# Performance work log

Hardware: AMD Instinct MI355X
Metric: run time of the kernel (lower is better)

The kernel has to match this reference:

```python
import jax, jax.numpy as jnp
import numpy as np

L, D, H, DK, DV, DFF = 6, 512, 8, 64, 64, 2048
B, S = 8, 512
EPS = 1e-5


def _pos_table(max_len, d_model):
    pos = np.arange(max_len)[:, None].astype(np.float64)
    i = np.arange(d_model)[None, :].astype(np.float64)
    t = pos / np.power(10000.0, 2.0 * i / d_model)
    t[0, :] = 0.0
    t[1:, 0::2] = np.sin(t[1:, 0::2])
    t[1:, 1::2] = np.cos(t[1:, 1::2])
    return jnp.asarray(t, dtype=jnp.float32)


def _ln(x, g, b):
    m = jnp.mean(x, axis=-1, keepdims=True)
    v = jnp.mean(jnp.square(x - m), axis=-1, keepdims=True)
    return (x - m) * jax.lax.rsqrt(v + EPS) * g + b


def setup_inputs() -> dict:
    key = jax.random.key(0)
    ks = jax.random.split(key, 12)
    s = 0.02
    return {
        "enc_inputs": jax.random.normal(ks[0], (B, S, D), jnp.float32),
        "enc_inputs_mask": jax.random.randint(ks[1], (B, S), 0, 100, dtype=jnp.int64),
        "Wq": jax.random.normal(ks[2], (L, D, H * DK), jnp.float32) * s,
        "Wk": jax.random.normal(ks[3], (L, D, H * DK), jnp.float32) * s,
        "Wv": jax.random.normal(ks[4], (L, D, H * DV), jnp.float32) * s,
        "Wo": jax.random.normal(ks[5], (L, H * DV, D), jnp.float32) * s,
        "ln1_g": jnp.ones((L, D), jnp.float32),
        "ln1_b": jnp.zeros((L, D), jnp.float32),
        "W1": jax.random.normal(ks[6], (L, D, DFF), jnp.float32) * s,
        "W2": jax.random.normal(ks[7], (L, DFF, D), jnp.float32) * s,
        "ln2_g": jnp.ones((L, D), jnp.float32),
        "ln2_b": jnp.zeros((L, D), jnp.float32),
    }


def reference(enc_inputs, enc_inputs_mask, Wq, Wk, Wv, Wo, ln1_g, ln1_b, W1, W2, ln2_g, ln2_b):
    b, s, _ = enc_inputs.shape
    x = enc_inputs + _pos_table(s, D)  # positional encoding (dropout = eval/no-op)
    # pad mask: True where key token is pad (mask id == 0); broadcast over heads & queries
    pad = (enc_inputs_mask == 0)[:, None, None, :]  # [B,1,1,S]
    inv_sqrt_dk = np.float32(1.0 / np.sqrt(DK))
    attns = []
    for l in range(L):
        residual = x
        q = (x @ Wq[l]).reshape(b, s, H, DK).transpose(0, 2, 1, 3)  # [B,H,S,DK]
        k = (x @ Wk[l]).reshape(b, s, H, DK).transpose(0, 2, 1, 3)
        v = (x @ Wv[l]).reshape(b, s, H, DV).transpose(0, 2, 1, 3)
        scores = jnp.einsum("bhqd,bhkd->bhqk", q, k) * inv_sqrt_dk
        scores = jnp.where(pad, jnp.float32(-1e9), scores)
        attn = jax.nn.softmax(scores, axis=-1)
        ctx = jnp.einsum("bhqk,bhkd->bhqd", attn, v)
        ctx = ctx.transpose(0, 2, 1, 3).reshape(b, s, H * DV)
        x = _ln(ctx @ Wo[l] + residual, ln1_g[l], ln1_b[l])
        x = _ln(jax.nn.relu(x @ W1[l]) @ W2[l] + x, ln2_g[l], ln2_b[l])
        attns.append(attn)
    return x, jnp.stack(attns)  # [B,S,D], [L,B,H,S,S]
```

## Files before the change

kernel.cpp:

```cpp
#include <hip/hip_runtime.h>

typedef __attribute__((ext_vector_type(8))) short bf16x8;
typedef __attribute__((ext_vector_type(4))) short bf16x4;
typedef __attribute__((ext_vector_type(4))) float f32x4;

__device__ __forceinline__ float b2f(ushort u) {
  union { uint u; float f; } x; x.u = ((uint)u) << 16; return x.f;
}
__device__ __forceinline__ ushort f2b(float f) {
  union { float f; uint u; } x; x.f = f;
  uint r = x.u + 0x7fffu + ((x.u >> 16) & 1u);
  return (ushort)(r >> 16);
}
__device__ __forceinline__ f32x4 mfma16(bf16x8 a, bf16x8 b, f32x4 c) {
  return __builtin_amdgcn_mfma_f32_16x16x32_bf16(a, b, c, 0, 0, 0);
}
__device__ __forceinline__ void glds16(const ushort* g, ushort* l) {
  __builtin_amdgcn_global_load_lds((const __attribute__((address_space(1))) void*)g,
                                   (__attribute__((address_space(3))) void*)l, 16, 0, 0);
}
#define VMCNT0 asm volatile("s_waitcnt vmcnt(0)" ::: "memory")

__global__ void detect_kernel(const uint* __restrict__ ln1g, const uint* __restrict__ mask,
                              int* __restrict__ flags) {
  if (threadIdx.x == 0) {
    flags[0] = (ln1g[0] == 0x3F800000u) ? 1 : 0;
    int odd0 = 1;
    for (int i = 0; i < 16; i++)
      if (mask[2 * i + 1] != 0u) odd0 = 0;
    flags[1] = odd0;
  }
}

__device__ __forceinline__ void convt_tile(const void* __restrict__ src, ushort* __restrict__ dst,
                                           int K, int N, int l, int k0, int n0, int f) {
  __shared__ ushort T[64][72];
  size_t mo = (size_t)l * K * N;
  int r = threadIdx.x >> 2, c = (threadIdx.x & 3) * 16;
  if (f) {
    const float* sp = (const float*)src + mo + (size_t)(k0 + r) * N + n0 + c;
#pragma unroll
    for (int i = 0; i < 16; i += 4) {
      float4 fv = *(const float4*)(sp + i);
      T[c + i][r] = f2b(fv.x); T[c + i + 1][r] = f2b(fv.y);
      T[c + i + 2][r] = f2b(fv.z); T[c + i + 3][r] = f2b(fv.w);
    }
  } else {
    const ushort* sp = (const ushort*)src + mo + (size_t)(k0 + r) * N + n0 + c;
    bf16x8 v0 = *(const bf16x8*)sp;
    bf16x8 v1 = *(const bf16x8*)(sp + 8);
#pragma unroll
    for (int i = 0; i < 8; i++) { T[c + i][r] = (ushort)v0[i]; T[c + 8 + i][r] = (ushort)v1[i]; }
  }
  __syncthreads();
  ushort* d = dst + mo + (size_t)(n0 + r) * K + k0 + c;
  *(bf16x8*)d = *(const bf16x8*)&T[r][c];
  *(bf16x8*)(d + 8) = *(const bf16x8*)&T[r][c + 8];
}

__global__ __launch_bounds__(256) void convt_all_kernel(
    const void* __restrict__ Wq, const void* __restrict__ Wk, const void* __restrict__ Wv,
    const void* __restrict__ Wo, const void* __restrict__ W1, const void* __restrict__ W2,
    ushort* __restrict__ tWq, ushort* __restrict__ tWk, ushort* __restrict__ tWv,
    ushort* __restrict__ tWo, ushort* __restrict__ tW1, ushort* __restrict__ tW2,
    const int* __restrict__ flags) {
  int f = flags[0];
  int id = blockIdx.x;
  if (id < 1536) {
    const void* s; ushort* d;
    if (id < 384)       { s = Wq; d = tWq; }
    else if (id < 768)  { s = Wk; d = tWk; id -= 384; }
    else if (id < 1152) { s = Wv; d = tWv; id -= 768; }
    else                { s = Wo; d = tWo; id -= 1152; }
    int l = id >> 6, rr = id & 63;
    convt_tile(s, d, 512, 512, l, (rr & 7) * 64, (rr >> 3) * 64, f);
  } else if (id < 3072) {
    int r = id - 1536;
    int l = r >> 8, rr = r & 255;
    convt_tile(W1, tW1, 512, 2048, l, (rr & 7) * 64, (rr >> 3) * 64, f);
  } else {
    int r = id - 3072;
    int l = r >> 8, rr = r & 255;
    convt_tile(W2, tW2, 2048, 512, l, (rr & 31) * 64, (rr >> 5) * 64, f);
  }
}

__global__ __launch_bounds__(256) void posadd_kernel(const void* __restrict__ enc,
                                                     float* __restrict__ x32,
                                                     ushort* __restrict__ xb,
                                                     const int* __restrict__ flags) {
  int f = flags[0];
  int idx = blockIdx.x * 256 + threadIdx.x;
  int s = idx >> 9, d = idx & 511;
  float pef = 0.f;
  if (s > 0) {
    double t = (double)s / pow(10000.0, 2.0 * (double)d / 512.0);
    pef = (float)((d & 1) ? cos(t) : sin(t));
  }
  for (int b = 0; b < 8; b++) {
    size_t o = ((size_t)(b * 512 + s)) * 512 + d;
    float ev = f ? ((const float*)enc)[o] : b2f(((const ushort*)enc)[o]);
    float xv = ev + pef;
    x32[o] = xv;
    xb[o] = f2b(xv);
  }
}

template <bool RELU, int OUTMODE>
__device__ __forceinline__ void gemm_bt_core(const ushort* __restrict__ A,
                                             const ushort* __restrict__ Bt,
                                             ushort* __restrict__ C,
                                             int M, int N, int K, int bm, int bn) {
  __shared__ ushort As[2 * 128 * 64];
  __shared__ ushort Bs[2 * 128 * 64];
  int tid = threadIdx.x;
  int wave = tid >> 6, lane = tid & 63;
  int lm = lane & 15, lq = lane >> 4;
  int wm = (wave & 1) * 64, wn = (wave >> 1) * 64;
  int m0 = bm * 128, n0 = bn * 128;
  f32x4 z = {0.f, 0.f, 0.f, 0.f};
  f32x4 acc[4][4];
#pragma unroll
  for (int mi = 0; mi < 4; mi++)
#pragma unroll
    for (int ni = 0; ni < 4; ni++) acc[mi][ni] = z;

  int sr = tid >> 3, sc = (tid & 7) * 8;
  const ushort* ap = A + (size_t)(m0 + sr) * K + sc;
  const ushort* bp = Bt + (size_t)(n0 + sr) * K + sc;
  int nt = K >> 6;

#pragma unroll
  for (int j = 0; j < 4; j++) {
    glds16(ap + (size_t)(j * 32) * K, As + tid * 8 + j * 2048);
    glds16(bp + (size_t)(j * 32) * K, Bs + tid * 8 + j * 2048);
  }
  VMCNT0;
  __builtin_amdgcn_s_barrier();
  __builtin_amdgcn_sched_barrier(0);

  for (int t = 0; t < nt; t++) {
    int cur = (t & 1) * 8192;
    if (t + 1 < nt) {
      int nxt = ((t + 1) & 1) * 8192;
      int k0 = (t + 1) << 6;
#pragma unroll
      for (int j = 0; j < 4; j++) {
        glds16(ap + (size_t)(j * 32) * K + k0, As + nxt + tid * 8 + j * 2048);
        glds16(bp + (size_t)(j * 32) * K + k0, Bs + nxt + tid * 8 + j * 2048);
      }
    }
#pragma unroll
    for (int kk = 0; kk < 64; kk += 32) {
      bf16x8 af[4], bfv[4];
#pragma unroll
      for (int mi = 0; mi < 4; mi++)
        af[mi] = *(const bf16x8*)&As[cur + (wm + mi * 16 + lm) * 64 + kk + lq * 8];
#pragma unroll
      for (int ni = 0; ni < 4; ni++)
        bfv[ni] = *(const bf16x8*)&Bs[cur + (wn + ni * 16 + lm) * 64 + kk + lq * 8];
#pragma unroll
      for (int mi = 0; mi < 4; mi++)
#pragma unroll
        for (int ni = 0; ni < 4; ni++)
          acc[mi][ni] = mfma16(af[mi], bfv[ni], acc[mi][ni]);
    }
    VMCNT0;
    __builtin_amdgcn_s_barrier();
    __builtin_amdgcn_sched_barrier(0);
  }

  if (OUTMODE == 0) {
#pragma unroll
    for (int mi = 0; mi < 4; mi++)
#pragma unroll
      for (int ni = 0; ni < 4; ni++) {
        int row = m0 + wm + mi * 16 + lq * 4;
        int col = n0 + wn + ni * 16 + lm;
#pragma unroll
        for (int r = 0; r < 4; r++) {
          float vv = acc[mi][ni][r];
          if (RELU) vv = fmaxf(vv, 0.f);
          C[(size_t)(row + r) * N + col] = f2b(vv);
        }
      }
  } else {
#pragma unroll
    for (int mi = 0; mi < 4; mi++)
#pragma unroll
      for (int ni = 0; ni < 4; ni++) {
        int row = m0 + wm + mi * 16 + lq * 4;
        int col = n0 + wn + ni * 16 + lm;
        int b = row >> 9, s = row & 511;
        bf16x4 o;
#pragma unroll
        for (int r = 0; r < 4; r++) o[r] = (short)f2b(acc[mi][ni][r]);
        *(bf16x4*)&C[((size_t)(b * 8 + (col >> 6)) * 64 + (col & 63)) * 512 + s] = o;
      }
  }
}

template <bool RELU>
__global__ __launch_bounds__(256) void gemm_bt_kernel(const ushort* __restrict__ A,
                                                      const ushort* __restrict__ Bt,
                                                      ushort* __restrict__ C, int M, int N, int K) {
  gemm_bt_core<RELU, 0>(A, Bt, C, M, N, K, blockIdx.x, blockIdx.y);
}

template <bool RELU, int OUTMODE>
__device__ __forceinline__ void gemm64_core(const ushort* __restrict__ A,
                                            const ushort* __restrict__ Bt,
                                            ushort* __restrict__ C,
                                            int M, int N, int K, int bm, int bn) {
  __shared__ ushort As[2 * 64 * 64];
  __shared__ ushort Bs[2 * 64 * 64];
  int tid = threadIdx.x;
  int wave = tid >> 6, lane = tid & 63;
  int lm = lane & 15, lq = lane >> 4;
  int wm = (wave & 1) * 32, wn = (wave >> 1) * 32;
  int m0 = bm * 64, n0 = bn * 64;
  f32x4 z = {0.f, 0.f, 0.f, 0.f};
  f32x4 acc[2][2];
#pragma unroll
  for (int mi = 0; mi < 2; mi++)
#pragma unroll
    for (int ni = 0; ni < 2; ni++) acc[mi][ni] = z;

  int sr = tid >> 3, sc = (tid & 7) * 8;
  const ushort* ap = A + (size_t)(m0 + sr) * K + sc;
  const ushort* bp = Bt + (size_t)(n0 + sr) * K + sc;
  int nt = K >> 6;

#pragma unroll
  for (int j = 0; j < 2; j++) {
    glds16(ap + (size_t)(j * 32) * K, As + tid * 8 + j * 2048);
    glds16(bp + (size_t)(j * 32) * K, Bs + tid * 8 + j * 2048);
  }
  VMCNT0;
  __builtin_amdgcn_s_barrier();
  __builtin_amdgcn_sched_barrier(0);

  for (int t = 0; t < nt; t++) {
    int cur = (t & 1) * 4096;
    if (t + 1 < nt) {
      int nxt = ((t + 1) & 1) * 4096;
      int k0 = (t + 1) << 6;
#pragma unroll
      for (int j = 0; j < 2; j++) {
        glds16(ap + (size_t)(j * 32) * K + k0, As + nxt + tid * 8 + j * 2048);
        glds16(bp + (size_t)(j * 32) * K + k0, Bs + nxt + tid * 8 + j * 2048);
      }
    }
#pragma unroll
    for (int kk = 0; kk < 64; kk += 32) {
      bf16x8 af[2], bfv[2];
#pragma unroll
      for (int mi = 0; mi < 2; mi++)
        af[mi] = *(const bf16x8*)&As[cur + (wm + mi * 16 + lm) * 64 + kk + lq * 8];
#pragma unroll
      for (int ni = 0; ni < 2; ni++)
        bfv[ni] = *(const bf16x8*)&Bs[cur + (wn + ni * 16 + lm) * 64 + kk + lq * 8];
#pragma unroll
      for (int mi = 0; mi < 2; mi++)
#pragma unroll
        for (int ni = 0; ni < 2; ni++)
          acc[mi][ni] = mfma16(af[mi], bfv[ni], acc[mi][ni]);
    }
    VMCNT0;
    __builtin_amdgcn_s_barrier();
    __builtin_amdgcn_sched_barrier(0);
  }

  if (OUTMODE == 0) {
#pragma unroll
    for (int mi = 0; mi < 2; mi++)
#pragma unroll
      for (int ni = 0; ni < 2; ni++) {
        int row = m0 + wm + mi * 16 + lq * 4;
        int col = n0 + wn + ni * 16 + lm;
#pragma unroll
        for (int r = 0; r < 4; r++) {
          float vv = acc[mi][ni][r];
          if (RELU) vv = fmaxf(vv, 0.f);
          C[(size_t)(row + r) * N + col] = f2b(vv);
        }
      }
  } else {
#pragma unroll
    for (int mi = 0; mi < 2; mi++)
#pragma unroll
      for (int ni = 0; ni < 2; ni++) {
        int row = m0 + wm + mi * 16 + lq * 4;
        int col = n0 + wn + ni * 16 + lm;
        int b = row >> 9, s = row & 511;
        bf16x4 o;
#pragma unroll
        for (int r = 0; r < 4; r++) o[r] = (short)f2b(acc[mi][ni][r]);
        *(bf16x4*)&C[((size_t)(b * 8 + (col >> 6)) * 64 + (col & 63)) * 512 + s] = o;
      }
  }
}

template <bool RELU>
__global__ __launch_bounds__(256) void gemm64_kernel(const ushort* __restrict__ A,
                                                     const ushort* __restrict__ Bt,
                                                     ushort* __restrict__ C, int M, int N, int K) {
  gemm64_core<RELU, 0>(A, Bt, C, M, N, K, blockIdx.x, blockIdx.y);
}

__global__ __launch_bounds__(256) void gemm64_qkv_kernel(const ushort* __restrict__ A,
                                                         const ushort* __restrict__ Wq,
                                                         const ushort* __restrict__ Wk,
                                                         const ushort* __restrict__ Wv,
                                                         ushort* __restrict__ q, ushort* __restrict__ k,
                                                         ushort* __restrict__ vt, int M, int N, int K) {
  if (blockIdx.z == 0)      gemm64_core<false, 0>(A, Wq, q,  M, N, K, blockIdx.x, blockIdx.y);
  else if (blockIdx.z == 1) gemm64_core<false, 0>(A, Wk, k,  M, N, K, blockIdx.x, blockIdx.y);
  else                      gemm64_core<false, 1>(A, Wv, vt, M, N, K, blockIdx.x, blockIdx.y);
}

__global__ __launch_bounds__(256) void gemm64sk_kernel(const ushort* __restrict__ A,
                                                       const ushort* __restrict__ Bt,
                                                       float* __restrict__ Cp,
                                                       int M, int N, int K) {
  __shared__ ushort As[2 * 64 * 64];
  __shared__ ushort Bs[2 * 64 * 64];
  int kh = K >> 1;
  int sk = blockIdx.z;
  const ushort* Ab = A + (size_t)sk * kh;
  const ushort* Bb = Bt + (size_t)sk * kh;
  float* C = Cp + (size_t)sk * M * N;
  int tid = threadIdx.x;
  int wave = tid >> 6, lane = tid & 63;
  int lm = lane & 15, lq = lane >> 4;
  int wm = (wave & 1) * 32, wn = (wave >> 1) * 32;
  int m0 = blockIdx.x * 64, n0 = blockIdx.y * 64;
  f32x4 z = {0.f, 0.f, 0.f, 0.f};
  f32x4 acc[2][2];
#pragma unroll
  for (int mi = 0; mi < 2; mi++)
#pragma unroll
    for (int ni = 0; ni < 2; ni++) acc[mi][ni] = z;

  int sr = tid >> 3, sc = (tid & 7) * 8;
  const ushort* ap = Ab + (size_t)(m0 + sr) * K + sc;
  const ushort* bp = Bb + (size_t)(n0 + sr) * K + sc;
  int nt = kh >> 6;

#pragma unroll
  for (int j = 0; j < 2; j++) {
    glds16(ap + (size_t)(j * 32) * K, As + tid * 8 + j * 2048);
    glds16(bp + (size_t)(j * 32) * K, Bs + tid * 8 + j * 2048);
  }
  VMCNT0;
  __builtin_amdgcn_s_barrier();
  __builtin_amdgcn_sched_barrier(0);

  for (int t = 0; t < nt; t++) {
    int cur = (t & 1) * 4096;
    if (t + 1 < nt) {
      int nxt = ((t + 1) & 1) * 4096;
      int k0 = (t + 1) << 6;
#pragma unroll
      for (int j = 0; j < 2; j++) {
        glds16(ap + (size_t)(j * 32) * K + k0, As + nxt + tid * 8 + j * 2048);
        glds16(bp + (size_t)(j * 32) * K + k0, Bs + nxt + tid * 8 + j * 2048);
      }
    }
#pragma unroll
    for (int kk = 0; kk < 64; kk += 32) {
      bf16x8 af[2], bfv[2];
#pragma unroll
      for (int mi = 0; mi < 2; mi++)
        af[mi] = *(const bf16x8*)&As[cur + (wm + mi * 16 + lm) * 64 + kk + lq * 8];
#pragma unroll
      for (int ni = 0; ni < 2; ni++)
        bfv[ni] = *(const bf16x8*)&Bs[cur + (wn + ni * 16 + lm) * 64 + kk + lq * 8];
#pragma unroll
      for (int mi = 0; mi < 2; mi++)
#pragma unroll
        for (int ni = 0; ni < 2; ni++)
          acc[mi][ni] = mfma16(af[mi], bfv[ni], acc[mi][ni]);
    }
    VMCNT0;
    __builtin_amdgcn_s_barrier();
    __builtin_amdgcn_sched_barrier(0);
  }

#pragma unroll
  for (int mi = 0; mi < 2; mi++)
#pragma unroll
    for (int ni = 0; ni < 2; ni++) {
      int row = m0 + wm + mi * 16 + lq * 4;
      int col = n0 + wn + ni * 16 + lm;
#pragma unroll
      for (int r = 0; r < 4; r++)
        C[(size_t)(row + r) * N + col] = acc[mi][ni][r];
    }
}

__global__ __launch_bounds__(256) void attn_kernel(const ushort* __restrict__ qb, const ushort* __restrict__ kb,
                                                   const ushort* __restrict__ vt, const uint* __restrict__ mask,
                                                   void* __restrict__ out_base, size_t out_elem_off,
                                                   ushort* __restrict__ ctx, const int* __restrict__ flags) {
  __shared__ ushort Qs[16][72];
  __shared__ float maskf[512];
  __shared__ float redm[4][16];
  __shared__ float reds[4][16];
  __shared__ ushort Pb[16 * 512];
  int of32 = flags[0], m64 = flags[1];
  int tid = threadIdx.x, wave = tid >> 6, lane = tid & 63;
  int lm = lane & 15, lq = lane >> 4;
  int wg = blockIdx.x;
  int slot = wg >> 3;
  int bh = (wg & 7) + 8 * (slot >> 5);
  int b = bh >> 3, h = bh & 7;
  int q0 = (slot & 31) * 16;
  {
    int r = tid >> 4, c = (tid & 15) * 4;
    const ushort* src = qb + (size_t)(b * 512 + q0 + r) * 512 + h * 64 + c;
    *(bf16x4*)&Qs[r][c] = *(const bf16x4*)src;
  }
  {
#pragma unroll
    for (int i = 0; i < 2; i++) {
      int kk = tid * 2 + i;
      uint mv = mask[(size_t)(b * 512 + kk) << m64];
      maskf[kk] = (mv == 0u) ? -1e9f : 0.f;
    }
  }
  __syncthreads();
  bf16x8 a0 = *(const bf16x8*)&Qs[lm][lq * 8];
  bf16x8 a1 = *(const bf16x8*)&Qs[lm][32 + lq * 8];
  f32x4 z = {0.f, 0.f, 0.f, 0.f};
  f32x4 acc[8];
#pragma unroll
  for (int t8 = 0; t8 < 8; t8++) {
    int key = (wave * 8 + t8) * 16 + lm;
    const ushort* kp = kb + (size_t)(b * 512 + key) * 512 + h * 64;
    bf16x8 kb0 = *(const bf16x8*)(kp + lq * 8);
    bf16x8 kb1 = *(const bf16x8*)(kp + 32 + lq * 8);
    f32x4 s = mfma16(a0, kb0, z);
    s = mfma16(a1, kb1, s);
    float mf = maskf[key];
#pragma unroll
    for (int r = 0; r < 4; r++) acc[t8][r] = s[r] * 0.125f + mf;
  }
  float rmax[4];
#pragma unroll
  for (int r = 0; r < 4; r++) {
    float v = acc[0][r];
#pragma unroll
    for (int t8 = 1; t8 < 8; t8++) v = fmaxf(v, acc[t8][r]);
    v = fmaxf(v, __shfl_xor(v, 1));
    v = fmaxf(v, __shfl_xor(v, 2));
    v = fmaxf(v, __shfl_xor(v, 4));
    v = fmaxf(v, __shfl_xor(v, 8));
    rmax[r] = v;
  }
  if (lm == 0) {
#pragma unroll
    for (int r = 0; r < 4; r++) redm[wave][lq * 4 + r] = rmax[r];
  }
  __syncthreads();
#pragma unroll
  for (int r = 0; r < 4; r++) {
    int row = lq * 4 + r;
    rmax[r] = fmaxf(fmaxf(redm[0][row], redm[1][row]), fmaxf(redm[2][row], redm[3][row]));
  }
  float rsum[4];
#pragma unroll
  for (int r = 0; r < 4; r++) {
    float s = 0.f;
#pragma unroll
    for (int t8 = 0; t8 < 8; t8++) {
      float e = expf(acc[t8][r] - rmax[r]);
      acc[t8][r] = e;
      s += e;
    }
    s += __shfl_xor(s, 1);
    s += __shfl_xor(s, 2);
    s += __shfl_xor(s, 4);
    s += __shfl_xor(s, 8);
    rsum[r] = s;
  }
  if (lm == 0) {
#pragma unroll
    for (int r = 0; r < 4; r++) reds[wave][lq * 4 + r] = rsum[r];
  }
  __syncthreads();
  float rinv[4];
#pragma unroll
  for (int r = 0; r < 4; r++) {
    int row = lq * 4 + r;
    rinv[r] = 1.f / (reds[0][row] + reds[1][row] + reds[2][row] + reds[3][row]);
  }
  if (of32) {
    float* ao = (float*)out_base;
#pragma unroll
    for (int t8 = 0; t8 < 8; t8++)
#pragma unroll
      for (int r = 0; r < 4; r++) {
        int row = lq * 4 + r, key = (wave * 8 + t8) * 16 + lm;
        float pf = acc[t8][r] * rinv[r];
        Pb[(row * 512 + key) ^ ((row & 7) << 3)] = f2b(pf);
        ao[out_elem_off + ((size_t)(b * 8 + h) * 512 + q0 + row) * 512 + key] = pf;
      }
  } else {
    ushort* ao = (ushort*)out_base;
#pragma unroll
    for (int t8 = 0; t8 < 8; t8++)
#pragma unroll
      for (int r = 0; r < 4; r++) {
        int row = lq * 4 + r, key = (wave * 8 + t8) * 16 + lm;
        ushort pb = f2b(acc[t8][r] * rinv[r]);
        Pb[(row * 512 + key) ^ ((row & 7) << 3)] = pb;
        ao[out_elem_off + ((size_t)(b * 8 + h) * 512 + q0 + row) * 512 + key] = pb;
      }
  }
  __syncthreads();
  f32x4 c = z;
  int d = wave * 16 + lm;
  const ushort* vp = vt + ((size_t)bh * 64 + d) * 512;
#pragma unroll 4
  for (int ks = 0; ks < 16; ks++) {
    bf16x8 pa = *(const bf16x8*)&Pb[(lm * 512 + ks * 32 + lq * 8) ^ ((lm & 7) << 3)];
    bf16x8 bv = *(const bf16x8*)(vp + ks * 32 + lq * 8);
    c = mfma16(pa, bv, c);
  }
#pragma unroll
  for (int r = 0; r < 4; r++) {
    ctx[(size_t)(b * 512 + q0 + lq * 4 + r) * 512 + h * 64 + d] = f2b(c[r]);
  }
}

__global__ __launch_bounds__(256) void ln_kernel(const ushort* __restrict__ a, float* __restrict__ x32,
                                                 ushort* __restrict__ xb, const void* __restrict__ g,
                                                 const void* __restrict__ bb, int goff,
                                                 const int* __restrict__ flags, void* __restrict__ fout,
                                                 const float* __restrict__ pa0,
                                                 const float* __restrict__ pa1) {
  int f = flags[0];
  int row = blockIdx.x, tid = threadIdx.x;
  size_t base = (size_t)row * 512;
  float a0v, a1v;
  if (pa0) {
    a0v = pa0[base + tid] + pa1[base + tid];
    a1v = pa0[base + tid + 256] + pa1[base + tid + 256];
  } else {
    a0v = b2f(a[base + tid]);
    a1v = b2f(a[base + tid + 256]);
  }
  float v0 = a0v + x32[base + tid];
  float v1 = a1v + x32[base + tid + 256];
  float s1 = v0 + v1, s2 = v0 * v0 + v1 * v1;
#pragma unroll
  for (int off = 32; off > 0; off >>= 1) {
    s1 += __shfl_down(s1, off);
    s2 += __shfl_down(s2, off);
  }
  __shared__ float r1[4], r2[4];
  if ((tid & 63) == 0) { r1[tid >> 6] = s1; r2[tid >> 6] = s2; }
  __syncthreads();
  s1 = r1[0] + r1[1] + r1[2] + r1[3];
  s2 = r2[0] + r2[1] + r2[2] + r2[3];
  float m = s1 * (1.f / 512.f);
  float var = s2 * (1.f / 512.f) - m * m;
  float rs = rsqrtf(var + 1e-5f);
  float g0, g1v, b0, b1;
  if (f) {
    const float* gp = (const float*)g + goff;
    const float* bp = (const float*)bb + goff;
    g0 = gp[tid]; g1v = gp[tid + 256]; b0 = bp[tid]; b1 = bp[tid + 256];
  } else {
    const ushort* gp = (const ushort*)g + goff;
    const ushort* bp = (const ushort*)bb + goff;
    g0 = b2f(gp[tid]); g1v = b2f(gp[tid + 256]); b0 = b2f(bp[tid]); b1 = b2f(bp[tid + 256]);
  }
  float y0 = (v0 - m) * rs * g0 + b0;
  float y1 = (v1 - m) * rs * g1v + b1;
  if (fout) {
    if (f) {
      ((float*)fout)[base + tid] = y0;
      ((float*)fout)[base + tid + 256] = y1;
    } else {
      ((ushort*)fout)[base + tid] = f2b(y0);
      ((ushort*)fout)[base + tid + 256] = f2b(y1);
    }
  } else {
    x32[base + tid] = y0;        xb[base + tid] = f2b(y0);
    x32[base + tid + 256] = y1;  xb[base + tid + 256] = f2b(y1);
  }
}

extern "C" void kernel_launch(void* const* d_in, const int* in_sizes, int n_in,
                              void* d_out, int out_size, void* d_ws, size_t ws_size,
                              hipStream_t stream) {
  const void* enc  = d_in[0];
  const uint* mask = (const uint*)d_in[1];
  const void* Wq   = d_in[2];
  const void* Wk   = d_in[3];
  const void* Wv   = d_in[4];
  const void* Wo   = d_in[5];
  const void* ln1g = d_in[6];
  const void* ln1b = d_in[7];
  const void* W1   = d_in[8];
  const void* W2   = d_in[9];
  const void* ln2g = d_in[10];
  const void* ln2b = d_in[11];

  char* p = (char*)d_ws;
  int* flags  = (int*)p;      p += 256;
  ushort* tWq = (ushort*)p;   p += (size_t)1572864 * 2;
  ushort* tWk = (ushort*)p;   p += (size_t)1572864 * 2;
  ushort* tWv = (ushort*)p;   p += (size_t)1572864 * 2;
  ushort* tWo = (ushort*)p;   p += (size_t)1572864 * 2;
  ushort* tW1 = (ushort*)p;   p += (size_t)6291456 * 2;
  ushort* tW2 = (ushort*)p;   p += (size_t)6291456 * 2;
  float*  x32 = (float*)p;    p += (size_t)2097152 * 4;
  ushort* xb  = (ushort*)p;   p += (size_t)2097152 * 2;
  ushort* g2  = (ushort*)p;   p += (size_t)2097152 * 2;
  ushort* ctx = (ushort*)p;   p += (size_t)2097152 * 2;
  ushort* q   = (ushort*)p;   p += (size_t)2097152 * 2;
  ushort* k   = (ushort*)p;   p += (size_t)2097152 * 2;
  p += (size_t)2097152 * 2;
  ushort* vt  = (ushort*)p;   p += (size_t)2097152 * 2;
  float* g2p  = (float*)p;    p += (size_t)2 * 2097152 * 4;
  ushort* g1  = q;

  detect_kernel<<<1, 64, 0, stream>>>((const uint*)ln1g, mask, flags);
  convt_all_kernel<<<4608, 256, 0, stream>>>(Wq, Wk, Wv, Wo, W1, W2,
                                             tWq, tWk, tWv, tWo, tW1, tW2, flags);
  posadd_kernel<<<1024, 256, 0, stream>>>(enc, x32, xb, flags);

  for (int l = 0; l < 6; l++) {
    gemm64_qkv_kernel<<<dim3(64, 8, 3), 256, 0, stream>>>(
        xb, tWq + (size_t)l * 262144, tWk + (size_t)l * 262144, tWv + (size_t)l * 262144,
        q, k, vt, 4096, 512, 512);
    attn_kernel<<<2048, 256, 0, stream>>>(
        q, k, vt, mask, d_out, (size_t)2097152 + (size_t)l * 16777216, ctx, flags);
    gemm64_kernel<false><<<dim3(64, 8), 256, 0, stream>>>(ctx, tWo + (size_t)l * 262144, g2, 4096, 512, 512);
    ln_kernel<<<4096, 256, 0, stream>>>(g2, x32, xb, ln1g, ln1b, l * 512, flags, nullptr,
                                        nullptr, nullptr);
    gemm_bt_kernel<true><<<dim3(32, 16), 256, 0, stream>>>(xb, tW1 + (size_t)l * 1048576, g1, 4096, 2048, 512);
    gemm64sk_kernel<<<dim3(64, 8, 2), 256, 0, stream>>>(g1, tW2 + (size_t)l * 1048576, g2p, 4096, 512, 2048);
    ln_kernel<<<4096, 256, 0, stream>>>(g2, x32, xb, ln2g, ln2b, l * 512, flags,
                                        l == 5 ? d_out : nullptr, g2p, g2p + (size_t)2097152);
  }
}
```

Baseline: 1.209 ms.

## Split-K the Wo GEMM, fold posadd into weight convert, shrink mask smem

```diff
diff --git a/kernel.cpp b/kernel.cpp
--- a/kernel.cpp
+++ b/kernel.cpp
@@ -63,9 +63,28 @@
     const void* __restrict__ Wo, const void* __restrict__ W1, const void* __restrict__ W2,
     ushort* __restrict__ tWq, ushort* __restrict__ tWk, ushort* __restrict__ tWv,
     ushort* __restrict__ tWo, ushort* __restrict__ tW1, ushort* __restrict__ tW2,
+    const void* __restrict__ enc, float* __restrict__ x32, ushort* __restrict__ xb,
     const int* __restrict__ flags) {
   int f = flags[0];
   int id = blockIdx.x;
+  if (id >= 4608) {
+    int pid = id - 4608;
+    int idx = pid * 256 + threadIdx.x;
+    int s = idx >> 9, d = idx & 511;
+    float pef = 0.f;
+    if (s > 0) {
+      double t = (double)s / pow(10000.0, 2.0 * (double)d / 512.0);
+      pef = (float)((d & 1) ? cos(t) : sin(t));
+    }
+    for (int b = 0; b < 8; b++) {
+      size_t o = ((size_t)(b * 512 + s)) * 512 + d;
+      float ev = f ? ((const float*)enc)[o] : b2f(((const ushort*)enc)[o]);
+      float xv = ev + pef;
+      x32[o] = xv;
+      xb[o] = f2b(xv);
+    }
+    return;
+  }
   if (id < 1536) {
     const void* s; ushort* d;
     if (id < 384)       { s = Wq; d = tWq; }
@@ -82,27 +101,6 @@
     int r = id - 3072;
     int l = r >> 8, rr = r & 255;
     convt_tile(W2, tW2, 2048, 512, l, (rr & 31) * 64, (rr >> 5) * 64, f);
-  }
-}
-
-__global__ __launch_bounds__(256) void posadd_kernel(const void* __restrict__ enc,
-                                                     float* __restrict__ x32,
-                                                     ushort* __restrict__ xb,
-                                                     const int* __restrict__ flags) {
-  int f = flags[0];
-  int idx = blockIdx.x * 256 + threadIdx.x;
-  int s = idx >> 9, d = idx & 511;
-  float pef = 0.f;
-  if (s > 0) {
-    double t = (double)s / pow(10000.0, 2.0 * (double)d / 512.0);
-    pef = (float)((d & 1) ? cos(t) : sin(t));
-  }
-  for (int b = 0; b < 8; b++) {
-    size_t o = ((size_t)(b * 512 + s)) * 512 + d;
-    float ev = f ? ((const float*)enc)[o] : b2f(((const ushort*)enc)[o]);
-    float xv = ev + pef;
-    x32[o] = xv;
-    xb[o] = f2b(xv);
   }
 }
 
@@ -301,13 +299,6 @@
   }
 }
 
-template <bool RELU>
-__global__ __launch_bounds__(256) void gemm64_kernel(const ushort* __restrict__ A,
-                                                     const ushort* __restrict__ Bt,
-                                                     ushort* __restrict__ C, int M, int N, int K) {
-  gemm64_core<RELU, 0>(A, Bt, C, M, N, K, blockIdx.x, blockIdx.y);
-}
-
 __global__ __launch_bounds__(256) void gemm64_qkv_kernel(const ushort* __restrict__ A,
                                                          const ushort* __restrict__ Wq,
                                                          const ushort* __restrict__ Wk,
@@ -322,10 +313,9 @@
 __global__ __launch_bounds__(256) void gemm64sk_kernel(const ushort* __restrict__ A,
                                                        const ushort* __restrict__ Bt,
                                                        float* __restrict__ Cp,
-                                                       int M, int N, int K) {
+                                                       int M, int N, int K, int kh) {
   __shared__ ushort As[2 * 64 * 64];
   __shared__ ushort Bs[2 * 64 * 64];
-  int kh = K >> 1;
   int sk = blockIdx.z;
   const ushort* Ab = A + (size_t)sk * kh;
   const ushort* Bb = Bt + (size_t)sk * kh;
@@ -404,7 +394,7 @@
                                                    void* __restrict__ out_base, size_t out_elem_off,
                                                    ushort* __restrict__ ctx, const int* __restrict__ flags) {
   __shared__ ushort Qs[16][72];
-  __shared__ float maskf[512];
+  __shared__ ushort maskb[512];
   __shared__ float redm[4][16];
   __shared__ float reds[4][16];
   __shared__ ushort Pb[16 * 512];
@@ -426,7 +416,7 @@
     for (int i = 0; i < 2; i++) {
       int kk = tid * 2 + i;
       uint mv = mask[(size_t)(b * 512 + kk) << m64];
-      maskf[kk] = (mv == 0u) ? -1e9f : 0.f;
+      maskb[kk] = (mv == 0u) ? f2b(-1e9f) : (ushort)0;
     }
   }
   __syncthreads();
@@ -442,7 +432,7 @@
     bf16x8 kb1 = *(const bf16x8*)(kp + 32 + lq * 8);
     f32x4 s = mfma16(a0, kb0, z);
     s = mfma16(a1, kb1, s);
-    float mf = maskf[key];
+    float mf = b2f(maskb[key]);
 #pragma unroll
     for (int r = 0; r < 4; r++) acc[t8][r] = s[r] * 0.125f + mf;
   }
@@ -629,9 +619,9 @@
   ushort* g1  = q;
 
   detect_kernel<<<1, 64, 0, stream>>>((const uint*)ln1g, mask, flags);
-  convt_all_kernel<<<4608, 256, 0, stream>>>(Wq, Wk, Wv, Wo, W1, W2,
-                                             tWq, tWk, tWv, tWo, tW1, tW2, flags);
-  posadd_kernel<<<1024, 256, 0, stream>>>(enc, x32, xb, flags);
+  convt_all_kernel<<<5632, 256, 0, stream>>>(Wq, Wk, Wv, Wo, W1, W2,
+                                             tWq, tWk, tWv, tWo, tW1, tW2,
+                                             enc, x32, xb, flags);
 
   for (int l = 0; l < 6; l++) {
     gemm64_qkv_kernel<<<dim3(64, 8, 3), 256, 0, stream>>>(
@@ -639,11 +629,13 @@
         q, k, vt, 4096, 512, 512);
     attn_kernel<<<2048, 256, 0, stream>>>(
         q, k, vt, mask, d_out, (size_t)2097152 + (size_t)l * 16777216, ctx, flags);
-    gemm64_kernel<false><<<dim3(64, 8), 256, 0, stream>>>(ctx, tWo + (size_t)l * 262144, g2, 4096, 512, 512);
+    gemm64sk_kernel<<<dim3(64, 8, 2), 256, 0, stream>>>(
+        ctx, tWo + (size_t)l * 262144, g2p, 4096, 512, 512, 256);
     ln_kernel<<<4096, 256, 0, stream>>>(g2, x32, xb, ln1g, ln1b, l * 512, flags, nullptr,
-                                        nullptr, nullptr);
+                                        g2p, g2p + (size_t)2097152);
     gemm_bt_kernel<true><<<dim3(32, 16), 256, 0, stream>>>(xb, tW1 + (size_t)l * 1048576, g1, 4096, 2048, 512);
-    gemm64sk_kernel<<<dim3(64, 8, 2), 256, 0, stream>>>(g1, tW2 + (size_t)l * 1048576, g2p, 4096, 512, 2048);
+    gemm64sk_kernel<<<dim3(64, 8, 2), 256, 0, stream>>>(
+        g1, tW2 + (size_t)l * 1048576, g2p, 4096, 512, 2048, 1024);
     ln_kernel<<<4096, 256, 0, stream>>>(g2, x32, xb, ln2g, ln2b, l * 512, flags,
                                         l == 5 ? d_out : nullptr, g2p, g2p + (size_t)2097152);
   }
```

Result: no change. 1.218 ms (+0.8%).
